# Performance work log

Measured on AMD Instinct MI355X. Metric: run time of the kernel, lower is better.

Reference implementation:

```python
import jax, jax.numpy as jnp
import numpy as np

H, KVH, D = 32, 8, 128            # query heads, kv heads, head dim
HIDDEN = H * D                     # 4096
B, S = 32, 2048                    # decode batch, max kv length
THETA = 10000.0
SCALE = D ** -0.5


def setup_inputs() -> dict:
    key = jax.random.key(0)
    ks = jax.random.split(key, 6)
    return {
        "hidden_states": jax.random.normal(ks[0], (B, HIDDEN), jnp.float32),
        "w_qkv": jax.random.normal(ks[1], ((H + 2 * KVH) * D, HIDDEN), jnp.float32) * (HIDDEN ** -0.5),
        "w_o": jax.random.normal(ks[2], (HIDDEN, HIDDEN), jnp.float32) * (HIDDEN ** -0.5),
        "k_cache": jax.random.normal(ks[3], (B, S, KVH, D), jnp.float32),
        "v_cache": jax.random.normal(ks[4], (B, S, KVH, D), jnp.float32),
        "positions": jax.random.randint(ks[5], (B,), 0, S, jnp.int32),
    }


def _rope(x, positions):
    # x: [B, nheads, D], neox-style rotary over full head dim
    half = D // 2
    inv_freq = 1.0 / (THETA ** (jnp.arange(0, half, dtype=jnp.float32) / half))
    freqs = positions.astype(jnp.float32)[:, None] * inv_freq[None, :]   # [B, half]
    cos = jnp.cos(freqs)[:, None, :]
    sin = jnp.sin(freqs)[:, None, :]
    x1, x2 = x[..., :half], x[..., half:]
    return jnp.concatenate([x1 * cos - x2 * sin, x2 * cos + x1 * sin], axis=-1)


def reference(hidden_states, w_qkv, w_o, k_cache, v_cache, positions):
    G = H // KVH  # query heads per kv head
    qkv = hidden_states @ w_qkv.T                      # [B, (H+2*KVH)*D]
    q, k, v = jnp.split(qkv, [H * D, (H + KVH) * D], axis=-1)
    q = _rope(q.reshape(B, H, D), positions)           # [B, H, D]
    k = _rope(k.reshape(B, KVH, D), positions)         # [B, KVH, D]
    v = v.reshape(B, KVH, D)

    # write current token's k/v into the cache at its position (paged-cache write)
    slot = (jnp.arange(S)[None, :] == positions[:, None])[:, :, None, None]  # [B,S,1,1]
    keys = jnp.where(slot, k[:, None], k_cache)        # [B, S, KVH, D]
    vals = jnp.where(slot, v[:, None], v_cache)

    qg = q.reshape(B, KVH, G, D)
    scores = jnp.einsum("bkgd,bskd->bkgs", qg, keys) * SCALE   # [B, KVH, G, S]
    valid = (jnp.arange(S)[None, :] <= positions[:, None])[:, None, None, :]
    scores = jnp.where(valid, scores, -jnp.inf)
    probs = jax.nn.softmax(scores, axis=-1)
    attn = jnp.einsum("bkgs,bskd->bkgd", probs, vals).reshape(B, H * D)
    return attn @ w_o.T                                # [B, HIDDEN]
```

## Files before the change

kernel.cpp:

```cpp
#include <hip/hip_runtime.h>
#include <hip/hip_bf16.h>

#define NH   32
#define NKVH 8
#define NG   4
#define DD   128
#define HID  4096
#define NQKV 6144
#define NB   32
#define SS   2048
#define SCALE 0.08838834764831845f
#define CHUNK 128
#define NCHUNK 16
#define QSPLIT 8
#define OSPLIT 16

typedef __attribute__((ext_vector_type(4))) float f32x4;
typedef __attribute__((ext_vector_type(8))) short bf16x8;
typedef __attribute__((ext_vector_type(4))) unsigned int u32x4;

#define OFF_QKVP  0u
#define OFF_QR    1572864u
#define OFF_KR    1703936u
#define OFF_VB    1736704u
#define OFF_PART  1769472u
#define OFF_ABF   3899392u
#define OFF_OPART 3964928u

static __device__ __forceinline__ unsigned short f2bf(float f) {
    __hip_bfloat16 h = __float2bfloat16(f);
    return __builtin_bit_cast(unsigned short, h);
}

static __device__ __forceinline__ unsigned int pack_bf16(float a, float b) {
    unsigned int ua = __builtin_bit_cast(unsigned int, a) + 0x8000u;
    unsigned int ub = __builtin_bit_cast(unsigned int, b) + 0x8000u;
    return __builtin_amdgcn_perm(ub, ua, 0x07060302u);
}

__global__ __launch_bounds__(256) void g_qkv(
    const float* __restrict__ hs, const float* __restrict__ w_qkv,
    float* __restrict__ qkv_part) {
    int tid = threadIdx.x;
    int wave = tid >> 6, lane = tid & 63, l16 = lane & 15, kgrp = lane >> 4;
    int j0 = (blockIdx.x * 4 + wave) * 16;
    int ks = blockIdx.y;
    const int K = HID, Kslice = HID / QSPLIT;
    int kbeg = ks * Kslice;

    f32x4 acc0 = {0.f,0.f,0.f,0.f}, acc1 = {0.f,0.f,0.f,0.f};
    const float* ar0 = hs + (size_t)l16 * K;
    const float* ar1 = hs + (size_t)(16 + l16) * K;
    const float* wr  = w_qkv + (size_t)(j0 + l16) * K;

#pragma unroll 4
    for (int k = kbeg; k < kbeg + Kslice; k += 32) {
        int kk = k + kgrp * 8;
        f32x4 a00 = *(const f32x4*)(ar0 + kk), a01 = *(const f32x4*)(ar0 + kk + 4);
        f32x4 a10 = *(const f32x4*)(ar1 + kk), a11 = *(const f32x4*)(ar1 + kk + 4);
        f32x4 w0  = *(const f32x4*)(wr  + kk), w1  = *(const f32x4*)(wr  + kk + 4);
        u32x4 pa0, pa1, pw;
        pa0[0] = pack_bf16(a00[0], a00[1]); pa0[1] = pack_bf16(a00[2], a00[3]);
        pa0[2] = pack_bf16(a01[0], a01[1]); pa0[3] = pack_bf16(a01[2], a01[3]);
        pa1[0] = pack_bf16(a10[0], a10[1]); pa1[1] = pack_bf16(a10[2], a10[3]);
        pa1[2] = pack_bf16(a11[0], a11[1]); pa1[3] = pack_bf16(a11[2], a11[3]);
        pw[0]  = pack_bf16(w0[0],  w0[1]);  pw[1]  = pack_bf16(w0[2],  w0[3]);
        pw[2]  = pack_bf16(w1[0],  w1[1]);  pw[3]  = pack_bf16(w1[2],  w1[3]);
        bf16x8 bw = __builtin_bit_cast(bf16x8, pw);
        acc0 = __builtin_amdgcn_mfma_f32_16x16x32_bf16(__builtin_bit_cast(bf16x8, pa0), bw, acc0, 0, 0, 0);
        acc1 = __builtin_amdgcn_mfma_f32_16x16x32_bf16(__builtin_bit_cast(bf16x8, pa1), bw, acc1, 0, 0, 0);
    }
    float* dst = qkv_part + (size_t)ks * 32 * NQKV + j0 + l16;
#pragma unroll
    for (int r = 0; r < 4; ++r) {
        dst[(size_t)(kgrp * 4 + r) * NQKV] = acc0[r];
        dst[(size_t)(16 + kgrp * 4 + r) * NQKV] = acc1[r];
    }
}

__global__ __launch_bounds__(256) void g_rope(
    const float* __restrict__ qkv_part, const int* __restrict__ positions,
    float* __restrict__ q_rope, float* __restrict__ k_rope, float* __restrict__ vbuf) {
    int idx = blockIdx.x * 256 + threadIdx.x;
    const int NROPE = NB * 40 * 64;
    const int NV = NB * NKVH * DD;
    if (idx < NROPE) {
        int i = idx & 63, head = (idx >> 6) % 40, b = idx / (64 * 40);
        size_t base = (size_t)b * NQKV + head * DD;
        float x1 = 0.f, x2 = 0.f;
#pragma unroll
        for (int p = 0; p < QSPLIT; ++p) {
            x1 += qkv_part[(size_t)p * 32 * NQKV + base + i];
            x2 += qkv_part[(size_t)p * 32 * NQKV + base + i + 64];
        }
        float pos = (float)positions[b];
        float inv = exp2f(-(float)i * 0.20762050593046f);
        float fr = pos * inv, s, c;
        sincosf(fr, &s, &c);
        float o1 = x1 * c - x2 * s, o2 = x2 * c + x1 * s;
        if (head < NH) {
            float* d = q_rope + ((size_t)b * NH + head) * DD;
            d[i] = o1; d[i + 64] = o2;
        } else {
            float* d = k_rope + ((size_t)b * NKVH + (head - NH)) * DD;
            d[i] = o1; d[i + 64] = o2;
        }
    } else if (idx < NROPE + NV) {
        int j = idx - NROPE;
        size_t base = (size_t)(j >> 10) * NQKV + (NH + NKVH) * DD + (j & 1023);
        float v = 0.f;
#pragma unroll
        for (int p = 0; p < QSPLIT; ++p) v += qkv_part[(size_t)p * 32 * NQKV + base];
        vbuf[j] = v;
    }
}

__global__ __launch_bounds__(256) void g_attn(
    const float* __restrict__ k_cache, const float* __restrict__ v_cache,
    const float* __restrict__ q_rope, const float* __restrict__ k_rope,
    const float* __restrict__ vbuf, const int* __restrict__ positions,
    float* __restrict__ part) {
    int bk = blockIdx.x;
    int c = blockIdx.y;
    int b = bk >> 3, kvh = bk & 7;
    int pos = positions[b];
    int s0 = c * CHUNK;
    float* mypart = part + ((size_t)bk * NCHUNK + c) * 520;
    int tid = threadIdx.x;
    if (s0 > pos) {
        if (tid < 4) { mypart[tid] = -__builtin_inff(); mypart[4 + tid] = 0.f; }
        return;
    }
    int nvalid = min(pos + 1 - s0, CHUNK);

    __shared__ float sc[4][CHUNK];
    __shared__ float mg[4], lg[4];
    __shared__ f32x4 red2[8][4][32];

    int wave = tid >> 6, lane = tid & 63, l16 = lane & 15, rsub = lane >> 4;

    for (int i = tid; i < 4 * CHUNK; i += 256) ((float*)sc)[i] = -__builtin_inff();
    __syncthreads();

    float qf[4][8];
    const float* qbase = q_rope + ((size_t)b * NH + kvh * NG) * DD;
#pragma unroll
    for (int g = 0; g < 4; ++g)
#pragma unroll
        for (int e = 0; e < 8; ++e)
            qf[g][e] = qbase[g * DD + l16 * 8 + e];

    const float* kcb = k_cache + ((size_t)b * SS * NKVH + kvh) * DD;
    const float* krp = k_rope + ((size_t)b * NKVH + kvh) * DD;

    if (nvalid == CHUNK) {
#pragma unroll
        for (int it = 0; it < CHUNK / 16; ++it) {
            int row = it * 16 + wave * 4 + rsub;
            int s = s0 + row;
            const float* krow = (s == pos) ? krp : (kcb + (size_t)s * (NKVH * DD));
            f32x4 k0 = *(const f32x4*)(krow + l16 * 8);
            f32x4 k1 = *(const f32x4*)(krow + l16 * 8 + 4);
            float dots[4];
#pragma unroll
            for (int g = 0; g < 4; ++g)
                dots[g] = qf[g][0]*k0[0] + qf[g][1]*k0[1] + qf[g][2]*k0[2] + qf[g][3]*k0[3]
                        + qf[g][4]*k1[0] + qf[g][5]*k1[1] + qf[g][6]*k1[2] + qf[g][7]*k1[3];
#pragma unroll
            for (int m = 1; m < 16; m <<= 1)
#pragma unroll
                for (int g = 0; g < 4; ++g)
                    dots[g] += __shfl_xor(dots[g], m, 64);
            if (l16 == 0)
#pragma unroll
                for (int g = 0; g < 4; ++g) sc[g][row] = dots[g] * SCALE;
        }
    } else {
#pragma unroll 2
        for (int it = 0; it < CHUNK / 16; ++it) {
            int row = it * 16 + wave * 4 + rsub;
            if (row >= nvalid) continue;
            int s = s0 + row;
            const float* krow = (s == pos) ? krp : (kcb + (size_t)s * (NKVH * DD));
            f32x4 k0 = *(const f32x4*)(krow + l16 * 8);
            f32x4 k1 = *(const f32x4*)(krow + l16 * 8 + 4);
            float dots[4];
#pragma unroll
            for (int g = 0; g < 4; ++g)
                dots[g] = qf[g][0]*k0[0] + qf[g][1]*k0[1] + qf[g][2]*k0[2] + qf[g][3]*k0[3]
                        + qf[g][4]*k1[0] + qf[g][5]*k1[1] + qf[g][6]*k1[2] + qf[g][7]*k1[3];
#pragma unroll
            for (int m = 1; m < 16; m <<= 1)
#pragma unroll
                for (int g = 0; g < 4; ++g)
                    dots[g] += __shfl_xor(dots[g], m, 64);
            if (l16 == 0)
#pragma unroll
                for (int g = 0; g < 4; ++g) sc[g][row] = dots[g] * SCALE;
        }
    }
    __syncthreads();

    {
        int g = wave;
        float v0 = sc[g][lane], v1 = sc[g][lane + 64];
        float m = fmaxf(v0, v1);
#pragma unroll
        for (int msk = 1; msk < 64; msk <<= 1) m = fmaxf(m, __shfl_xor(m, msk, 64));
        float p0 = expf(v0 - m), p1 = expf(v1 - m);
        float l = p0 + p1;
#pragma unroll
        for (int msk = 1; msk < 64; msk <<= 1) l += __shfl_xor(l, msk, 64);
        sc[g][lane] = p0; sc[g][lane + 64] = p1;
        if (lane == 0) { mg[g] = m; lg[g] = l; }
    }
    __syncthreads();

    int sid = tid >> 5, l32 = tid & 31;
    f32x4 acc[4] = {{0.f,0.f,0.f,0.f},{0.f,0.f,0.f,0.f},{0.f,0.f,0.f,0.f},{0.f,0.f,0.f,0.f}};
    const float* vcb = v_cache + ((size_t)b * SS * NKVH + kvh) * DD;
    const float* vrp = vbuf + ((size_t)b * NKVH + kvh) * DD;
    if (nvalid == CHUNK) {
#pragma unroll 4
        for (int row = sid; row < CHUNK; row += 8) {
            int s = s0 + row;
            const float* vrow = (s == pos) ? vrp : (vcb + (size_t)s * (NKVH * DD));
            f32x4 v4 = *(const f32x4*)(vrow + l32 * 4);
#pragma unroll
            for (int g = 0; g < 4; ++g) acc[g] += sc[g][row] * v4;
        }
    } else {
#pragma unroll 2
        for (int row = sid; row < nvalid; row += 8) {
            int s = s0 + row;
            const float* vrow = (s == pos) ? vrp : (vcb + (size_t)s * (NKVH * DD));
            f32x4 v4 = *(const f32x4*)(vrow + l32 * 4);
#pragma unroll
            for (int g = 0; g < 4; ++g) acc[g] += sc[g][row] * v4;
        }
    }
#pragma unroll
    for (int g = 0; g < 4; ++g) red2[sid][g][l32] = acc[g];
    __syncthreads();
    if (tid < 128) {
        int g = tid >> 5, l = tid & 31;
        f32x4 s = red2[0][g][l];
#pragma unroll
        for (int w = 1; w < 8; ++w) s += red2[w][g][l];
        *(f32x4*)(mypart + 8 + g * DD + l * 4) = s;
        if (l == 0) { mypart[g] = mg[g]; mypart[4 + g] = lg[g]; }
    }
}

__global__ __launch_bounds__(256) void g_combine(
    const float* __restrict__ part, unsigned short* __restrict__ attn_bf) {
    int tid = threadIdx.x;
    int bk = blockIdx.x * 2 + (tid >> 7);
    int t = tid & 127;
    int b = bk >> 3, kvh = bk & 7;
    const float* p0 = part + (size_t)bk * NCHUNK * 520;
    int g = t >> 5, l32 = t & 31;

    float M = -__builtin_inff();
#pragma unroll
    for (int c = 0; c < NCHUNK; ++c) {
        float lcv = p0[c * 520 + 4 + g];
        float mcv = p0[c * 520 + g];
        if (lcv > 0.f && mcv > M) M = mcv;
    }
    float L = 0.f;
    f32x4 acc = {0.f, 0.f, 0.f, 0.f};
#pragma unroll
    for (int c = 0; c < NCHUNK; ++c) {
        float lcv = p0[c * 520 + 4 + g];
        float mcv = p0[c * 520 + g];
        if (lcv > 0.f) {
            float wgt = expf(mcv - M);
            L += lcv * wgt;
            f32x4 a = *(const f32x4*)(p0 + c * 520 + 8 + g * DD + l32 * 4);
            acc += wgt * a;
        }
    }
    float inv = 1.0f / L;
    unsigned short* o = attn_bf + (((size_t)b * NH) + kvh * NG + g) * DD + l32 * 4;
#pragma unroll
    for (int r = 0; r < 4; ++r) o[r] = f2bf(acc[r] * inv);
}

__global__ __launch_bounds__(256) void g_o(
    const unsigned short* __restrict__ attn_bf, const float* __restrict__ w_o,
    float* __restrict__ o_part) {
    int tid = threadIdx.x;
    int wave = tid >> 6, lane = tid & 63, l16 = lane & 15, kgrp = lane >> 4;
    int j0 = (blockIdx.x * 4 + wave) * 16;
    int ks = blockIdx.y;
    const int K = HID, Kslice = HID / OSPLIT;
    int kbeg = ks * Kslice;

    f32x4 acc0 = {0.f,0.f,0.f,0.f}, acc1 = {0.f,0.f,0.f,0.f};
    const unsigned short* ar0 = attn_bf + (size_t)l16 * K;
    const unsigned short* ar1 = attn_bf + (size_t)(16 + l16) * K;
    const float* wr = w_o + (size_t)(j0 + l16) * K;

#pragma unroll 4
    for (int k = kbeg; k < kbeg + Kslice; k += 32) {
        int kk = k + kgrp * 8;
        bf16x8 a0 = *(const bf16x8*)(ar0 + kk);
        bf16x8 a1 = *(const bf16x8*)(ar1 + kk);
        f32x4 w0 = *(const f32x4*)(wr + kk), w1 = *(const f32x4*)(wr + kk + 4);
        u32x4 pw;
        pw[0] = pack_bf16(w0[0], w0[1]); pw[1] = pack_bf16(w0[2], w0[3]);
        pw[2] = pack_bf16(w1[0], w1[1]); pw[3] = pack_bf16(w1[2], w1[3]);
        bf16x8 bw = __builtin_bit_cast(bf16x8, pw);
        acc0 = __builtin_amdgcn_mfma_f32_16x16x32_bf16(a0, bw, acc0, 0, 0, 0);
        acc1 = __builtin_amdgcn_mfma_f32_16x16x32_bf16(a1, bw, acc1, 0, 0, 0);
    }
    float* dst = o_part + (size_t)ks * 32 * HID + j0 + l16;
#pragma unroll
    for (int r = 0; r < 4; ++r) {
        dst[(size_t)(kgrp * 4 + r) * HID] = acc0[r];
        dst[(size_t)(16 + kgrp * 4 + r) * HID] = acc1[r];
    }
}

__global__ __launch_bounds__(64) void g_reduce_o(
    const float* __restrict__ o_part, float* __restrict__ out) {
    int idx = blockIdx.x * 64 + threadIdx.x;
    const f32x4* p = (const f32x4*)o_part;
    f32x4 s = p[idx];
#pragma unroll
    for (int k = 1; k < OSPLIT; ++k) s += p[idx + k * 32768];
    ((f32x4*)out)[idx] = s;
}

extern "C" void kernel_launch(void* const* d_in, const int* in_sizes, int n_in,
                              void* d_out, int out_size, void* d_ws, size_t ws_size,
                              hipStream_t stream) {
    const float* hs      = (const float*)d_in[0];
    const float* w_qkv   = (const float*)d_in[1];
    const float* w_o     = (const float*)d_in[2];
    const float* k_cache = (const float*)d_in[3];
    const float* v_cache = (const float*)d_in[4];
    const int*   positions = (const int*)d_in[5];
    float* out = (float*)d_out;
    float* wsf = (float*)d_ws;

    float* p_qkv_part = wsf + OFF_QKVP;
    float* p_q_rope   = wsf + OFF_QR;
    float* p_k_rope   = wsf + OFF_KR;
    float* p_vbuf     = wsf + OFF_VB;
    float* p_part     = wsf + OFF_PART;
    unsigned short* p_attn_bf = (unsigned short*)(wsf + OFF_ABF);
    float* p_o_part   = wsf + OFF_OPART;

    hipLaunchKernelGGL(g_qkv, dim3(96, QSPLIT), dim3(256), 0, stream,
                       hs, w_qkv, p_qkv_part);
    hipLaunchKernelGGL(g_rope, dim3(448), dim3(256), 0, stream,
                       p_qkv_part, positions, p_q_rope, p_k_rope, p_vbuf);
    hipLaunchKernelGGL(g_attn, dim3(256, NCHUNK), dim3(256), 0, stream,
                       k_cache, v_cache, p_q_rope, p_k_rope, p_vbuf, positions, p_part);
    hipLaunchKernelGGL(g_combine, dim3(128), dim3(256), 0, stream,
                       p_part, p_attn_bf);
    hipLaunchKernelGGL(g_o, dim3(64, OSPLIT), dim3(256), 0, stream,
                       p_attn_bf, w_o, p_o_part);
    hipLaunchKernelGGL(g_reduce_o, dim3(512), dim3(64), 0, stream, p_o_part, out);
}
```

Before: 128.3 us.

## Process two KV heads per attention block with contiguous 1KB row loads

Each attention block now handles two adjacent KV heads (a 1KB contiguous slice of a cache row) instead of one. Each wave reads whole rows with 32 lanes per head, which halves the grid and gives more coalesced loads. A separate fast path for fully valid chunks skips the -inf initialisation and the per-row current-position check. The softmax and reduction stages are reorganised for eight heads per block, at the cost of longer 32-lane shuffle reductions and fewer blocks in flight.

```diff
diff --git a/kernel.cpp b/kernel.cpp
--- a/kernel.cpp
+++ b/kernel.cpp
@@ -120,135 +120,144 @@
     const float* __restrict__ q_rope, const float* __restrict__ k_rope,
     const float* __restrict__ vbuf, const int* __restrict__ positions,
     float* __restrict__ part) {
-    int bk = blockIdx.x;
+    int bx = blockIdx.x;
+    int b = bx >> 2, kp = bx & 3;
     int c = blockIdx.y;
-    int b = bk >> 3, kvh = bk & 7;
     int pos = positions[b];
     int s0 = c * CHUNK;
-    float* mypart = part + ((size_t)bk * NCHUNK + c) * 520;
     int tid = threadIdx.x;
     if (s0 > pos) {
-        if (tid < 4) { mypart[tid] = -__builtin_inff(); mypart[4 + tid] = 0.f; }
+        if (tid < 16) {
+            int k2 = tid >> 3, j = tid & 7;
+            float* rec = part + ((size_t)(b * NKVH + kp * 2 + k2) * NCHUNK + c) * 520;
+            rec[j] = (j < 4) ? -__builtin_inff() : 0.f;
+        }
         return;
     }
     int nvalid = min(pos + 1 - s0, CHUNK);
-
-    __shared__ float sc[4][CHUNK];
-    __shared__ float mg[4], lg[4];
-    __shared__ f32x4 red2[8][4][32];
-
-    int wave = tid >> 6, lane = tid & 63, l16 = lane & 15, rsub = lane >> 4;
-
-    for (int i = tid; i < 4 * CHUNK; i += 256) ((float*)sc)[i] = -__builtin_inff();
-    __syncthreads();
-
-    float qf[4][8];
-    const float* qbase = q_rope + ((size_t)b * NH + kvh * NG) * DD;
-#pragma unroll
-    for (int g = 0; g < 4; ++g)
-#pragma unroll
-        for (int e = 0; e < 8; ++e)
-            qf[g][e] = qbase[g * DD + l16 * 8 + e];
-
-    const float* kcb = k_cache + ((size_t)b * SS * NKVH + kvh) * DD;
-    const float* krp = k_rope + ((size_t)b * NKVH + kvh) * DD;
-
-    if (nvalid == CHUNK) {
-#pragma unroll
-        for (int it = 0; it < CHUNK / 16; ++it) {
-            int row = it * 16 + wave * 4 + rsub;
-            int s = s0 + row;
-            const float* krow = (s == pos) ? krp : (kcb + (size_t)s * (NKVH * DD));
-            f32x4 k0 = *(const f32x4*)(krow + l16 * 8);
-            f32x4 k1 = *(const f32x4*)(krow + l16 * 8 + 4);
+    bool clean = (pos >= s0 + CHUNK);
+
+    __shared__ float sc[2][4][CHUNK];
+    __shared__ float mg[8], lg[8];
+    __shared__ f32x4 red[4][8][33];
+
+    int wave = tid >> 6, lane = tid & 63;
+    int kvh2 = lane >> 5, l = lane & 31;
+    int kvh = kp * 2 + kvh2;
+    const int ROWST = NKVH * DD;
+
+    f32x4 qf[4];
+    const float* qb = q_rope + ((size_t)b * NH + kvh * NG) * DD + l * 4;
+#pragma unroll
+    for (int g = 0; g < 4; ++g) qf[g] = *(const f32x4*)(qb + g * DD);
+
+    const float* kcb = k_cache + (size_t)b * SS * ROWST;
+
+    if (clean) {
+        const float* kpp = kcb + (size_t)(s0 + wave) * ROWST + kvh * DD + l * 4;
+#pragma unroll 4
+        for (int it = 0; it < CHUNK / 4; ++it) {
+            f32x4 kv = *(const f32x4*)(kpp + (size_t)it * 4 * ROWST);
             float dots[4];
 #pragma unroll
             for (int g = 0; g < 4; ++g)
-                dots[g] = qf[g][0]*k0[0] + qf[g][1]*k0[1] + qf[g][2]*k0[2] + qf[g][3]*k0[3]
-                        + qf[g][4]*k1[0] + qf[g][5]*k1[1] + qf[g][6]*k1[2] + qf[g][7]*k1[3];
-#pragma unroll
-            for (int m = 1; m < 16; m <<= 1)
+                dots[g] = kv[0]*qf[g][0] + kv[1]*qf[g][1] + kv[2]*qf[g][2] + kv[3]*qf[g][3];
+#pragma unroll
+            for (int m = 1; m < 32; m <<= 1)
 #pragma unroll
                 for (int g = 0; g < 4; ++g)
                     dots[g] += __shfl_xor(dots[g], m, 64);
-            if (l16 == 0)
-#pragma unroll
-                for (int g = 0; g < 4; ++g) sc[g][row] = dots[g] * SCALE;
+            if (l == 0)
+#pragma unroll
+                for (int g = 0; g < 4; ++g) sc[kvh2][g][it * 4 + wave] = dots[g] * SCALE;
+        }
+    } else {
+        for (int i = tid; i < 2 * 4 * CHUNK; i += 256) ((float*)sc)[i] = -__builtin_inff();
+        __syncthreads();
+#pragma unroll 2
+        for (int it = 0; it < CHUNK / 4; ++it) {
+            int row = it * 4 + wave;
+            if (row >= nvalid) continue;
+            int s = s0 + row;
+            const float* kr = (s == pos)
+                ? (k_rope + ((size_t)b * NKVH + kvh) * DD)
+                : (kcb + (size_t)s * ROWST + kvh * DD);
+            f32x4 kv = *(const f32x4*)(kr + l * 4);
+            float dots[4];
+#pragma unroll
+            for (int g = 0; g < 4; ++g)
+                dots[g] = kv[0]*qf[g][0] + kv[1]*qf[g][1] + kv[2]*qf[g][2] + kv[3]*qf[g][3];
+#pragma unroll
+            for (int m = 1; m < 32; m <<= 1)
+#pragma unroll
+                for (int g = 0; g < 4; ++g)
+                    dots[g] += __shfl_xor(dots[g], m, 64);
+            if (l == 0)
+#pragma unroll
+                for (int g = 0; g < 4; ++g) sc[kvh2][g][row] = dots[g] * SCALE;
+        }
+    }
+    __syncthreads();
+
+    {
+        int head = tid >> 5;
+        int hk = head >> 2, hg = head & 3;
+        int t = tid & 31;
+        float v0 = sc[hk][hg][t], v1 = sc[hk][hg][t + 32],
+              v2 = sc[hk][hg][t + 64], v3 = sc[hk][hg][t + 96];
+        float m = fmaxf(fmaxf(v0, v1), fmaxf(v2, v3));
+#pragma unroll
+        for (int msk = 1; msk < 32; msk <<= 1) m = fmaxf(m, __shfl_xor(m, msk, 64));
+        float p0 = expf(v0 - m), p1 = expf(v1 - m), p2 = expf(v2 - m), p3 = expf(v3 - m);
+        float ls = p0 + p1 + p2 + p3;
+#pragma unroll
+        for (int msk = 1; msk < 32; msk <<= 1) ls += __shfl_xor(ls, msk, 64);
+        sc[hk][hg][t] = p0; sc[hk][hg][t + 32] = p1;
+        sc[hk][hg][t + 64] = p2; sc[hk][hg][t + 96] = p3;
+        if (t == 0) { mg[head] = m; lg[head] = ls; }
+    }
+    __syncthreads();
+
+    int dc = l;
+    f32x4 acc[4] = {{0.f,0.f,0.f,0.f},{0.f,0.f,0.f,0.f},{0.f,0.f,0.f,0.f},{0.f,0.f,0.f,0.f}};
+    const float* vcb = v_cache + (size_t)b * SS * ROWST;
+    if (clean) {
+        const float* vp = vcb + (size_t)(s0 + wave) * ROWST + kvh * DD + dc * 4;
+#pragma unroll 4
+        for (int it = 0; it < CHUNK / 4; ++it) {
+            f32x4 vv = *(const f32x4*)(vp + (size_t)it * 4 * ROWST);
+            int row = it * 4 + wave;
+#pragma unroll
+            for (int g = 0; g < 4; ++g) acc[g] += sc[kvh2][g][row] * vv;
         }
     } else {
 #pragma unroll 2
-        for (int it = 0; it < CHUNK / 16; ++it) {
-            int row = it * 16 + wave * 4 + rsub;
+        for (int it = 0; it < CHUNK / 4; ++it) {
+            int row = it * 4 + wave;
             if (row >= nvalid) continue;
             int s = s0 + row;
-            const float* krow = (s == pos) ? krp : (kcb + (size_t)s * (NKVH * DD));
-            f32x4 k0 = *(const f32x4*)(krow + l16 * 8);
-            f32x4 k1 = *(const f32x4*)(krow + l16 * 8 + 4);
-            float dots[4];
-#pragma unroll
-            for (int g = 0; g < 4; ++g)
-                dots[g] = qf[g][0]*k0[0] + qf[g][1]*k0[1] + qf[g][2]*k0[2] + qf[g][3]*k0[3]
-                        + qf[g][4]*k1[0] + qf[g][5]*k1[1] + qf[g][6]*k1[2] + qf[g][7]*k1[3];
-#pragma unroll
-            for (int m = 1; m < 16; m <<= 1)
-#pragma unroll
-                for (int g = 0; g < 4; ++g)
-                    dots[g] += __shfl_xor(dots[g], m, 64);
-            if (l16 == 0)
-#pragma unroll
-                for (int g = 0; g < 4; ++g) sc[g][row] = dots[g] * SCALE;
-        }
-    }
+            const float* vr = (s == pos)
+                ? (vbuf + ((size_t)b * NKVH + kvh) * DD)
+                : (vcb + (size_t)s * ROWST + kvh * DD);
+            f32x4 vv = *(const f32x4*)(vr + dc * 4);
+#pragma unroll
+            for (int g = 0; g < 4; ++g) acc[g] += sc[kvh2][g][row] * vv;
+        }
+    }
+#pragma unroll
+    for (int g = 0; g < 4; ++g) red[wave][kvh2 * 4 + g][dc] = acc[g];
     __syncthreads();
 
     {
-        int g = wave;
-        float v0 = sc[g][lane], v1 = sc[g][lane + 64];
-        float m = fmaxf(v0, v1);
-#pragma unroll
-        for (int msk = 1; msk < 64; msk <<= 1) m = fmaxf(m, __shfl_xor(m, msk, 64));
-        float p0 = expf(v0 - m), p1 = expf(v1 - m);
-        float l = p0 + p1;
-#pragma unroll
-        for (int msk = 1; msk < 64; msk <<= 1) l += __shfl_xor(l, msk, 64);
-        sc[g][lane] = p0; sc[g][lane + 64] = p1;
-        if (lane == 0) { mg[g] = m; lg[g] = l; }
-    }
-    __syncthreads();
-
-    int sid = tid >> 5, l32 = tid & 31;
-    f32x4 acc[4] = {{0.f,0.f,0.f,0.f},{0.f,0.f,0.f,0.f},{0.f,0.f,0.f,0.f},{0.f,0.f,0.f,0.f}};
-    const float* vcb = v_cache + ((size_t)b * SS * NKVH + kvh) * DD;
-    const float* vrp = vbuf + ((size_t)b * NKVH + kvh) * DD;
-    if (nvalid == CHUNK) {
-#pragma unroll 4
-        for (int row = sid; row < CHUNK; row += 8) {
-            int s = s0 + row;
-            const float* vrow = (s == pos) ? vrp : (vcb + (size_t)s * (NKVH * DD));
-            f32x4 v4 = *(const f32x4*)(vrow + l32 * 4);
-#pragma unroll
-            for (int g = 0; g < 4; ++g) acc[g] += sc[g][row] * v4;
-        }
-    } else {
-#pragma unroll 2
-        for (int row = sid; row < nvalid; row += 8) {
-            int s = s0 + row;
-            const float* vrow = (s == pos) ? vrp : (vcb + (size_t)s * (NKVH * DD));
-            f32x4 v4 = *(const f32x4*)(vrow + l32 * 4);
-#pragma unroll
-            for (int g = 0; g < 4; ++g) acc[g] += sc[g][row] * v4;
-        }
-    }
-#pragma unroll
-    for (int g = 0; g < 4; ++g) red2[sid][g][l32] = acc[g];
-    __syncthreads();
-    if (tid < 128) {
-        int g = tid >> 5, l = tid & 31;
-        f32x4 s = red2[0][g][l];
-#pragma unroll
-        for (int w = 1; w < 8; ++w) s += red2[w][g][l];
-        *(f32x4*)(mypart + 8 + g * DD + l * 4) = s;
-        if (l == 0) { mypart[g] = mg[g]; mypart[4 + g] = lg[g]; }
+        int k2 = tid >> 7, g = (tid >> 5) & 3, dc2 = tid & 31;
+        int h = k2 * 4 + g;
+        f32x4 s = red[0][h][dc2];
+        s += red[1][h][dc2];
+        s += red[2][h][dc2];
+        s += red[3][h][dc2];
+        float* rec = part + ((size_t)(b * NKVH + kp * 2 + k2) * NCHUNK + c) * 520;
+        *(f32x4*)(rec + 8 + g * DD + dc2 * 4) = s;
+        if (dc2 == 0) { rec[g] = mg[h]; rec[4 + g] = lg[h]; }
     }
 }
 
@@ -357,7 +366,7 @@
                        hs, w_qkv, p_qkv_part);
     hipLaunchKernelGGL(g_rope, dim3(448), dim3(256), 0, stream,
                        p_qkv_part, positions, p_q_rope, p_k_rope, p_vbuf);
-    hipLaunchKernelGGL(g_attn, dim3(256, NCHUNK), dim3(256), 0, stream,
+    hipLaunchKernelGGL(g_attn, dim3(NB * 4, NCHUNK), dim3(256), 0, stream,
                        k_cache, v_cache, p_q_rope, p_k_rope, p_vbuf, positions, p_part);
     hipLaunchKernelGGL(g_combine, dim3(128), dim3(256), 0, stream,
                        p_part, p_attn_bf);
```

After: 157.9 us. +23.1%, slower.
